# Performance work log

Measured on AMD Instinct MI355X. Metric: run time of the kernel, lower is better.

Reference implementation:

```python
import jax, jax.numpy as jnp
import numpy as np

WEIGHT_BITS = 8
INPUT_BITS = 8
HIDDEN = 4096
INTERMEDIATE = 16384
CLIP_INIT = 2.5


def _sym_quantize(x, clip_val, num_bits):
    """Symmetric layerwise uniform quantization with STE (PACT-style clip).

    Forward: clamp to [-clip, clip], round to 2^(b-1)-1 levels, dequantize.
    """
    clip_val = jnp.abs(clip_val)
    x_c = jnp.clip(x, -clip_val, clip_val)
    scale = clip_val / (2 ** (num_bits - 1) - 1)
    q = jnp.round(x_c / scale) * scale
    # straight-through estimator: gradient flows through the clamp only
    return x_c + jax.lax.stop_gradient(q - x_c)


def setup_inputs() -> dict:
    key = jax.random.key(0)
    k1, k2, k3 = jax.random.split(key, 3)
    hidden_states = jax.random.normal(k1, (2, 2048, HIDDEN), dtype=jnp.float32)
    # nn.Linear default init scale ~ 1/sqrt(fan_in)
    weight = jax.random.normal(k2, (INTERMEDIATE, HIDDEN), dtype=jnp.float32) / np.sqrt(HIDDEN)
    bias = jax.random.normal(k3, (INTERMEDIATE,), dtype=jnp.float32) * 0.01
    weight_clip_val = jnp.float32(CLIP_INIT)
    input_clip_val = jnp.float32(CLIP_INIT)
    return {
        "hidden_states": hidden_states,
        "weight": weight,
        "bias": bias,
        "weight_clip_val": weight_clip_val,
        "input_clip_val": input_clip_val,
    }


def reference(hidden_states, weight, bias, weight_clip_val, input_clip_val):
    wq = _sym_quantize(weight, weight_clip_val, WEIGHT_BITS)        # [I, H]
    xq = _sym_quantize(hidden_states, input_clip_val, INPUT_BITS)   # [B, S, H]
    out = jnp.einsum("bsh,ih->bsi", xq, wq) + bias                  # [B, S, I]
    return jax.nn.relu(out)
```

## Files before the change

kernel.cpp:

```cpp
#include <hip/hip_runtime.h>
#include <hip/hip_bf16.h>


#define HIDDEN 4096
#define INTER 16384
#define MDIM 4096

typedef int v4i __attribute__((ext_vector_type(4)));

__global__ __launch_bounds__(256) void quantize_kernel(
    const float* __restrict__ x,
    signed char* __restrict__ q,
    const float* __restrict__ clip_ptr,
    int n4)
{
    int i = blockIdx.x * blockDim.x + threadIdx.x;
    if (i >= n4) return;
    float c = fabsf(clip_ptr[0]);
    float inv_scale = 127.0f / c;
    float4 v = reinterpret_cast<const float4*>(x)[i];
    int q0 = __float2int_rn(fminf(fmaxf(v.x, -c), c) * inv_scale);
    int q1 = __float2int_rn(fminf(fmaxf(v.y, -c), c) * inv_scale);
    int q2 = __float2int_rn(fminf(fmaxf(v.z, -c), c) * inv_scale);
    int q3 = __float2int_rn(fminf(fmaxf(v.w, -c), c) * inv_scale);
    int pack = (q0 & 0xff) | ((q1 & 0xff) << 8) | ((q2 & 0xff) << 16) | (q3 << 24);
    reinterpret_cast<int*>(q)[i] = pack;
}

__global__ __launch_bounds__(256) void gemm_i8_kernel(
    const signed char* __restrict__ qA,
    const signed char* __restrict__ qB,
    const float* __restrict__ bias,
    const float* __restrict__ wclip,
    const float* __restrict__ iclip,
    float* __restrict__ out)
{
    __shared__ __align__(16) signed char As[128 * 128];
    __shared__ __align__(16) signed char Bs[128 * 128];

    const int t = threadIdx.x;
    const int W = t >> 6;
    const int L = t & 63;

    const int mBase = blockIdx.y * 128;
    const int nBase = blockIdx.x * 128;

    const int waveM = (W >> 1) * 64;
    const int waveN = (W & 1) * 64;

    v4i acc[4][4];
#pragma unroll
    for (int i = 0; i < 4; i++)
#pragma unroll
        for (int j = 0; j < 4; j++)
            acc[i][j] = (v4i){0, 0, 0, 0};

    const int sRow = W * 8 + (L >> 3);
    const int sCol = ((L & 7) ^ ((L >> 3) & 7)) * 16;
    const signed char* gA = qA + (size_t)(mBase + sRow) * HIDDEN + sCol;
    const signed char* gB = qB + (size_t)(nBase + sRow) * HIDDEN + sCol;
    const int ldsOff = W * 1024 + L * 16;

    const int lane16 = L & 15;
    const int quad = L >> 4;
    const int swz = (lane16 & 7);

    for (int k0 = 0; k0 < HIDDEN; k0 += 128) {
        __syncthreads();
#pragma unroll
        for (int i = 0; i < 4; i++) {
            __builtin_amdgcn_global_load_lds(
                (const __attribute__((address_space(1))) void*)(gA + (size_t)i * 32 * HIDDEN + k0),
                (__attribute__((address_space(3))) void*)(As + ldsOff + i * 4096),
                16, 0, 0);
            __builtin_amdgcn_global_load_lds(
                (const __attribute__((address_space(1))) void*)(gB + (size_t)i * 32 * HIDDEN + k0),
                (__attribute__((address_space(3))) void*)(Bs + ldsOff + i * 4096),
                16, 0, 0);
        }
        __syncthreads();

#pragma unroll
        for (int kk = 0; kk < 2; kk++) {
            v4i a[4], b[4];
#pragma unroll
            for (int tm = 0; tm < 4; tm++)
                a[tm] = *(const v4i*)(&As[(waveM + tm * 16 + lane16) * 128
                                          + (((kk * 4 + quad) ^ swz) * 16)]);
#pragma unroll
            for (int tn = 0; tn < 4; tn++)
                b[tn] = *(const v4i*)(&Bs[(waveN + tn * 16 + lane16) * 128
                                          + (((kk * 4 + quad) ^ swz) * 16)]);
#pragma unroll
            for (int tm = 0; tm < 4; tm++)
#pragma unroll
                for (int tn = 0; tn < 4; tn++)
                    acc[tm][tn] = __builtin_amdgcn_mfma_i32_16x16x64_i8(
                        a[tm], b[tn], acc[tm][tn], 0, 0, 0);
        }
    }

    const float scale = (fabsf(wclip[0]) / 127.0f) * (fabsf(iclip[0]) / 127.0f);

    float bv[4];
#pragma unroll
    for (int tn = 0; tn < 4; tn++)
        bv[tn] = bias[nBase + waveN + tn * 16 + lane16];

#pragma unroll
    for (int tm = 0; tm < 4; tm++) {
#pragma unroll
        for (int r = 0; r < 4; r++) {
            int m = mBase + waveM + tm * 16 + quad * 4 + r;
            float* orow = out + (size_t)m * INTER + nBase + waveN + lane16;
#pragma unroll
            for (int tn = 0; tn < 4; tn++) {
                float v = (float)acc[tm][tn][r] * scale + bv[tn];
                orow[tn * 16] = fmaxf(v, 0.0f);
            }
        }
    }
}

extern "C" void kernel_launch(void* const* d_in, const int* in_sizes, int n_in,
                              void* d_out, int out_size, void* d_ws, size_t ws_size,
                              hipStream_t stream) {
    const float* hidden_states  = (const float*)d_in[0];
    const float* weight         = (const float*)d_in[1];
    const float* bias           = (const float*)d_in[2];
    const float* weight_clip    = (const float*)d_in[3];
    const float* input_clip     = (const float*)d_in[4];
    float* out = (float*)d_out;

    signed char* qA = (signed char*)d_ws;
    signed char* qB = qA + (size_t)MDIM * HIDDEN;

    {
        int n4 = MDIM * HIDDEN / 4;
        quantize_kernel<<<n4 / 256, 256, 0, stream>>>(hidden_states, qA, input_clip, n4);
    }
    {
        int n4 = INTER * HIDDEN / 4;
        quantize_kernel<<<n4 / 256, 256, 0, stream>>>(weight, qB, weight_clip, n4);
    }

    dim3 grid(INTER / 128, MDIM / 128);
    gemm_i8_kernel<<<grid, 256, 0, stream>>>(qA, qB, bias, weight_clip, input_clip, out);
}
```

Baseline: 813.1 us.

## Rewrite int8 GEMM as 256x256 tile with double-buffered LDS pipeline

Replaces the 128x128 single-buffered int8 MFMA GEMM with a 256x256 tile per 512-thread block. Global-to-LDS loads are staged into double buffers ahead of use, with explicit vmcnt waits, raw barriers and setprio around MFMA quadrants so memory traffic overlaps compute. It also remaps block IDs for L2 locality. The bigger tile cuts global traffic per FLOP but uses 128KB of LDS and many accumulator registers, and the hand-tuned waitcnt and barrier schedule is fragile.

```diff
diff --git a/kernel.cpp b/kernel.cpp
--- a/kernel.cpp
+++ b/kernel.cpp
@@ -1,10 +1,11 @@
 #include <hip/hip_runtime.h>
-#include <hip/hip_bf16.h>
 
 
 #define HIDDEN 4096
 #define INTER 16384
 #define MDIM 4096
+#define BK 128
+#define NT (HIDDEN / BK)
 
 typedef int v4i __attribute__((ext_vector_type(4)));
 
@@ -27,7 +28,65 @@
     reinterpret_cast<int*>(q)[i] = pack;
 }
 
-__global__ __launch_bounds__(256) void gemm_i8_kernel(
+
+#define GLL(src, dst) __builtin_amdgcn_global_load_lds( \
+    (const __attribute__((address_space(1))) void*)(src), \
+    (__attribute__((address_space(3))) void*)(dst), 16, 0, 0)
+
+#define STAGE(gptr, lptr) do { \
+    GLL((gptr), (lptr)); \
+    GLL((gptr) + (size_t)64 * HIDDEN, (lptr) + 8192); } while (0)
+
+#define BARX() __builtin_amdgcn_s_barrier()
+#define LGKM0() asm volatile("s_waitcnt lgkmcnt(0)" ::: "memory")
+#define VM6() asm volatile("s_waitcnt vmcnt(6)" ::: "memory")
+#define VM4() asm volatile("s_waitcnt vmcnt(4)" ::: "memory")
+#define VM0() asm volatile("s_waitcnt vmcnt(0)" ::: "memory")
+#define VMNOP()
+#define PRIO1() __builtin_amdgcn_s_setprio(1)
+#define PRIO0() __builtin_amdgcn_s_setprio(0)
+
+#define READ_A(cb, qm) do { _Pragma("unroll") \
+    for (int m_ = 0; m_ < 4; m_++) { \
+      const signed char* p_ = &As[cb][(qm) * 16384 + aOff + m_ * 2048]; \
+      a[m_][0] = *reinterpret_cast<const v4i*>(p_ + c0); \
+      a[m_][1] = *reinterpret_cast<const v4i*>(p_ + c1); } } while (0)
+
+#define READ_B(cb, qn) do { _Pragma("unroll") \
+    for (int n_ = 0; n_ < 2; n_++) { \
+      const signed char* p_ = &Bs[cb][(qn) * 16384 + bOff + n_ * 2048]; \
+      b[n_][0] = *reinterpret_cast<const v4i*>(p_ + c0); \
+      b[n_][1] = *reinterpret_cast<const v4i*>(p_ + c1); } } while (0)
+
+#define MFMA_Q(qm, qn) do { _Pragma("unroll") \
+    for (int m_ = 0; m_ < 4; m_++) { _Pragma("unroll") \
+      for (int n_ = 0; n_ < 2; n_++) { \
+        acc[qm][qn][m_][n_] = __builtin_amdgcn_mfma_i32_16x16x64_i8( \
+            a[m_][0], b[n_][0], acc[qm][qn][m_][n_], 0, 0, 0); \
+        acc[qm][qn][m_][n_] = __builtin_amdgcn_mfma_i32_16x16x64_i8( \
+            a[m_][1], b[n_][1], acc[qm][qn][m_][n_], 0, 0, 0); } } } while (0)
+
+#define GROUP(cb, ob, T, SN, S2, VMW) do { \
+     \
+    READ_A(cb, 0); READ_B(cb, 0); \
+    if (SN) STAGE(gB + (size_t)((T) + 1) * BK, &Bs[ob][0] + ldsT); \
+    BARX(); LGKM0(); PRIO1(); MFMA_Q(0, 0); PRIO0(); BARX(); \
+     \
+    READ_B(cb, 1); \
+    if (S2) STAGE(gA + (size_t)((T) + 2) * BK, &As[cb][0] + ldsT); \
+    BARX(); LGKM0(); PRIO1(); MFMA_Q(0, 1); PRIO0(); BARX(); \
+     \
+    READ_A(cb, 1); \
+    if (S2) STAGE(gB + (size_t)128 * HIDDEN + (size_t)((T) + 2) * BK, &Bs[cb][16384] + ldsT); \
+    BARX(); LGKM0(); PRIO1(); MFMA_Q(1, 1); PRIO0(); BARX(); \
+     \
+    READ_B(cb, 0); \
+    if (S2) STAGE(gA + (size_t)128 * HIDDEN + (size_t)((T) + 2) * BK, &As[cb][16384] + ldsT); \
+    VMW(); \
+    BARX(); LGKM0(); PRIO1(); MFMA_Q(1, 0); PRIO0(); BARX(); \
+  } while (0)
+
+__global__ __launch_bounds__(512, 2) void gemm_i8_kernel(
     const signed char* __restrict__ qA,
     const signed char* __restrict__ qB,
     const float* __restrict__ bias,
@@ -35,91 +94,90 @@
     const float* __restrict__ iclip,
     float* __restrict__ out)
 {
-    __shared__ __align__(16) signed char As[128 * 128];
-    __shared__ __align__(16) signed char Bs[128 * 128];
+    __shared__ __align__(16) signed char As[2][32768];
+    __shared__ __align__(16) signed char Bs[2][32768];
 
     const int t = threadIdx.x;
+    const int L = t & 63;
     const int W = t >> 6;
-    const int L = t & 63;
-
-    const int mBase = blockIdx.y * 128;
-    const int nBase = blockIdx.x * 128;
-
-    const int waveM = (W >> 1) * 64;
-    const int waveN = (W & 1) * 64;
-
-    v4i acc[4][4];
-#pragma unroll
-    for (int i = 0; i < 4; i++)
-#pragma unroll
-        for (int j = 0; j < 4; j++)
-            acc[i][j] = (v4i){0, 0, 0, 0};
-
-    const int sRow = W * 8 + (L >> 3);
-    const int sCol = ((L & 7) ^ ((L >> 3) & 7)) * 16;
-    const signed char* gA = qA + (size_t)(mBase + sRow) * HIDDEN + sCol;
-    const signed char* gB = qB + (size_t)(nBase + sRow) * HIDDEN + sCol;
-    const int ldsOff = W * 1024 + L * 16;
-
+    const int wm = W >> 2;
+    const int wn = W & 3;
     const int lane16 = L & 15;
     const int quad = L >> 4;
-    const int swz = (lane16 & 7);
-
-    for (int k0 = 0; k0 < HIDDEN; k0 += 128) {
-        __syncthreads();
-#pragma unroll
-        for (int i = 0; i < 4; i++) {
-            __builtin_amdgcn_global_load_lds(
-                (const __attribute__((address_space(1))) void*)(gA + (size_t)i * 32 * HIDDEN + k0),
-                (__attribute__((address_space(3))) void*)(As + ldsOff + i * 4096),
-                16, 0, 0);
-            __builtin_amdgcn_global_load_lds(
-                (const __attribute__((address_space(1))) void*)(gB + (size_t)i * 32 * HIDDEN + k0),
-                (__attribute__((address_space(3))) void*)(Bs + ldsOff + i * 4096),
-                16, 0, 0);
-        }
-        __syncthreads();
-
-#pragma unroll
-        for (int kk = 0; kk < 2; kk++) {
-            v4i a[4], b[4];
-#pragma unroll
-            for (int tm = 0; tm < 4; tm++)
-                a[tm] = *(const v4i*)(&As[(waveM + tm * 16 + lane16) * 128
-                                          + (((kk * 4 + quad) ^ swz) * 16)]);
-#pragma unroll
-            for (int tn = 0; tn < 4; tn++)
-                b[tn] = *(const v4i*)(&Bs[(waveN + tn * 16 + lane16) * 128
-                                          + (((kk * 4 + quad) ^ swz) * 16)]);
-#pragma unroll
-            for (int tm = 0; tm < 4; tm++)
-#pragma unroll
-                for (int tn = 0; tn < 4; tn++)
-                    acc[tm][tn] = __builtin_amdgcn_mfma_i32_16x16x64_i8(
-                        a[tm], b[tn], acc[tm][tn], 0, 0, 0);
-        }
+    const int swz = lane16 & 7;
+
+    int wg = blockIdx.y * 64 + blockIdx.x;
+    wg = (wg & 7) * 128 + (wg >> 3);
+    const int mBase = (wg >> 6) * 256;
+    const int nBase = (wg & 63) * 256;
+
+    const int sRow = t >> 3;
+    const int sColSwz = ((t & 7) ^ (sRow & 7)) * 16;
+    const signed char* gA = qA + (size_t)(mBase + sRow) * HIDDEN + sColSwz;
+    const signed char* gB = qB + (size_t)(nBase + sRow) * HIDDEN + sColSwz;
+    const int ldsT = t * 16;
+
+    const int aOff = (wm * 64 + lane16) * 128;
+    const int bOff = (wn * 32 + lane16) * 128;
+    const int c0 = (quad ^ swz) * 16;
+    const int c1 = ((quad + 4) ^ swz) * 16;
+
+    v4i acc[2][2][4][2];
+#pragma unroll
+    for (int i = 0; i < 2; i++)
+#pragma unroll
+        for (int j = 0; j < 2; j++)
+#pragma unroll
+            for (int m = 0; m < 4; m++)
+#pragma unroll
+                for (int n = 0; n < 2; n++)
+                    acc[i][j][m][n] = (v4i){0, 0, 0, 0};
+
+    v4i a[4][2], b[2][2];
+
+    STAGE(gA, &As[0][0] + ldsT);
+    STAGE(gB, &Bs[0][0] + ldsT);
+    STAGE(gA + (size_t)128 * HIDDEN, &As[0][16384] + ldsT);
+    STAGE(gB + (size_t)128 * HIDDEN, &Bs[0][16384] + ldsT);
+    VM4();
+    STAGE(gA + BK, &As[1][0] + ldsT);
+    STAGE(gB + (size_t)128 * HIDDEN + BK, &Bs[1][16384] + ldsT);
+    STAGE(gA + (size_t)128 * HIDDEN + BK, &As[1][16384] + ldsT);
+    VM6();
+    BARX();
+
+    for (int T = 0; T < NT - 2; T += 2) {
+        GROUP(0, 1, T,     1, 1, VM6);
+        GROUP(1, 0, T + 1, 1, 1, VM6);
     }
+    GROUP(0, 1, NT - 2, 1, 0, VM0);
+    GROUP(1, 0, NT - 1, 0, 0, VMNOP);
 
     const float scale = (fabsf(wclip[0]) / 127.0f) * (fabsf(iclip[0]) / 127.0f);
 
-    float bv[4];
-#pragma unroll
-    for (int tn = 0; tn < 4; tn++)
-        bv[tn] = bias[nBase + waveN + tn * 16 + lane16];
-
-#pragma unroll
-    for (int tm = 0; tm < 4; tm++) {
-#pragma unroll
-        for (int r = 0; r < 4; r++) {
-            int m = mBase + waveM + tm * 16 + quad * 4 + r;
-            float* orow = out + (size_t)m * INTER + nBase + waveN + lane16;
-#pragma unroll
-            for (int tn = 0; tn < 4; tn++) {
-                float v = (float)acc[tm][tn][r] * scale + bv[tn];
-                orow[tn * 16] = fmaxf(v, 0.0f);
+    float bv[2][2];
+#pragma unroll
+    for (int qn = 0; qn < 2; qn++)
+#pragma unroll
+        for (int n = 0; n < 2; n++)
+            bv[qn][n] = bias[nBase + qn * 128 + wn * 32 + n * 16 + lane16];
+
+#pragma unroll
+    for (int qm = 0; qm < 2; qm++)
+#pragma unroll
+        for (int m = 0; m < 4; m++)
+#pragma unroll
+            for (int r = 0; r < 4; r++) {
+                const int row = mBase + qm * 128 + wm * 64 + m * 16 + quad * 4 + r;
+                float* orow = out + (size_t)row * INTER + nBase + wn * 32 + lane16;
+#pragma unroll
+                for (int qn = 0; qn < 2; qn++)
+#pragma unroll
+                    for (int n = 0; n < 2; n++) {
+                        float v = (float)acc[qm][qn][m][n][r] * scale + bv[qn][n];
+                        orow[qn * 128 + n * 16] = fmaxf(v, 0.0f);
+                    }
             }
-        }
-    }
 }
 
 extern "C" void kernel_launch(void* const* d_in, const int* in_sizes, int n_in,
@@ -144,6 +202,6 @@
         quantize_kernel<<<n4 / 256, 256, 0, stream>>>(weight, qB, weight_clip, n4);
     }
 
-    dim3 grid(INTER / 128, MDIM / 128);
-    gemm_i8_kernel<<<grid, 256, 0, stream>>>(qA, qB, bias, weight_clip, input_clip, out);
+    dim3 grid(INTER / 256, MDIM / 256);
+    gemm_i8_kernel<<<grid, 512, 0, stream>>>(qA, qB, bias, weight_clip, input_clip, out);
 }
```

Result: faster. 735.5 us (-9.5%).
